# Kernel tuning notes

Hardware: AMD Instinct MI355X
Metric: run time of the kernel (lower is better)

## Reference

```python
import jax, jax.numpy as jnp
import numpy as np

BS, L = 4096, 20
NF, EF, TF = 128, 128, 128
DM = 3 * NF + EF + TF          # 640: attention model dim
DIN = DM - TF                  # 512: GRU input dim
NHEAD = 2
NNODES, NEDGES = 100000, 500000
ODE_STEPS = 8


def setup_inputs() -> dict:
    key = jax.random.key(0)
    ks = jax.random.split(key, 32)
    p = lambda i, shape, s: jax.random.normal(ks[i], shape, dtype=jnp.float32) * s
    return {
        'nids': jax.random.randint(ks[0], (BS,), 1, NNODES),
        'ts': jax.random.uniform(ks[1], (BS,), dtype=jnp.float32),
        'hist_nids': jax.random.randint(ks[2], (BS, L), 0, NNODES),
        'anonymized_ids': jax.random.randint(ks[3], (BS, L), 0, L + 1),
        'hist_eids': jax.random.randint(ks[4], (BS, L), 0, NEDGES),
        'hist_ts': jnp.sort(jax.random.uniform(ks[5], (BS, L), dtype=jnp.float32), axis=1),
        'hist_dirs': jax.random.randint(ks[6], (BS, L), 0, 2),
        'node_feat': p(7, (NNODES, NF), 0.1),
        'edge_feat': p(8, (NEDGES, EF), 0.1),
        'anony_emb': p(9, (L + 1, NF), 0.1),
        'time_w': p(10, (TF,), 1.0),
        'time_b': p(11, (TF,), 1.0),
        'in_proj_w': p(12, (3 * DM, DM), 0.02),
        'in_proj_b': jnp.zeros((3 * DM,), jnp.float32),
        'out_proj_w': p(13, (DM, DM), 0.02),
        'out_proj_b': jnp.zeros((DM,), jnp.float32),
        'outfn_w': p(14, (NF, DM), 0.02),
        'outfn_b': jnp.zeros((NF,), jnp.float32),
        'attn_wq': p(15, (NF, NF), 0.05),
        'attn_wk': p(16, (NF + EF + TF, NF), 0.05),
        'attn_wv': p(17, (NF + EF + TF, NF), 0.05),
        'merge_w': p(18, (2 * NF, NF), 0.05),
        'merge_b': jnp.zeros((NF,), jnp.float32),
        'gru_w_ih': p(19, (3 * NF, DIN), 0.05),
        'gru_w_hh': p(20, (3 * NF, NF), 0.05),
        'gru_b_ih': jnp.zeros((3 * NF,), jnp.float32),
        'gru_b_hh': jnp.zeros((3 * NF,), jnp.float32),
        'ode_w': p(21, (NF, NF), 0.05),
        'ode_b': jnp.zeros((NF,), jnp.float32),
        'tnode_w': p(22, (NF,), 1.0),
        'tnode_b': p(23, (NF,), 1.0),
    }


def reference(nids, ts, hist_nids, anonymized_ids, hist_eids, hist_ts, hist_dirs,
              node_feat, edge_feat, anony_emb, time_w, time_b,
              in_proj_w, in_proj_b, out_proj_w, out_proj_b, outfn_w, outfn_b,
              attn_wq, attn_wk, attn_wv, merge_w, merge_b,
              gru_w_ih, gru_w_hh, gru_b_ih, gru_b_hh,
              ode_w, ode_b, tnode_w, tnode_b):
    bs, hl = hist_nids.shape
    mask = (hist_nids == 0)
    mask = mask.at[:, -1].set(False)
    invalid_rows = jnp.all(mask, axis=1, keepdims=True)  # [bs,1]

    r_nids = jnp.broadcast_to(nids[:, None], (bs, hl))
    src_nids = r_nids * hist_dirs + hist_nids * (1 - hist_dirs)
    dst_nids = r_nids * (1 - hist_dirs) + hist_nids * hist_dirs

    src_vals = node_feat[src_nids]                 # [bs,L,NF] gather
    dst_vals = node_feat[dst_nids]                 # [bs,L,NF] gather
    edge_vals = edge_feat[hist_eids]               # [bs,L,EF] gather
    anony_vals = anony_emb[anonymized_ids]         # [bs,L,NF] gather
    dt = hist_ts[:, -1:] - hist_ts                 # [bs,L]
    ts_vals = jnp.cos(dt[..., None] * time_w + time_b)  # [bs,L,TF] TimeEncode

    full_vals = jnp.concatenate([src_vals, dst_vals, anony_vals, edge_vals, ts_vals], axis=2)
    last_event_feat = full_vals[:, -1, :DIN]
    full_vals = full_vals.at[:, -1, :DIN].set(0.0)

    # --- self MHA over history (nn.MultiheadAttention with key_padding_mask) ---
    qkv = full_vals @ in_proj_w.T + in_proj_b      # [bs,L,3*DM]
    q, k, v = jnp.split(qkv, 3, axis=-1)
    dh = DM // NHEAD
    rs = lambda x: x.reshape(bs, hl, NHEAD, dh)
    scores = jnp.einsum('blhd,bmhd->bhlm', rs(q), rs(k)) / np.sqrt(dh)
    scores = jnp.where(mask[:, None, None, :], -1e9, scores)
    attn = jax.nn.softmax(scores, axis=-1)
    ctx = jnp.einsum('bhlm,bmhd->blhd', attn, rs(v)).reshape(bs, hl, DM)
    mha_out = ctx @ out_proj_w.T + out_proj_b

    # --- temporal graph attention embedding (GraphAttnEmbedding stand-in) ---
    qn = mha_out[:, -1] @ outfn_w.T + outfn_b      # [bs,NF]
    nb = jnp.concatenate([node_feat[hist_nids], edge_vals, ts_vals], axis=2)  # [bs,L,NF+EF+TF]
    qh = qn @ attn_wq                              # [bs,NF]
    kh = nb @ attn_wk                              # [bs,L,NF]
    vh = nb @ attn_wv                              # [bs,L,NF]
    sc = jnp.einsum('bd,bld->bl', qh, kh) / np.sqrt(NF)
    sc = jnp.where(mask, -1e9, sc)
    a = jax.nn.softmax(sc, axis=-1)
    ctx2 = jnp.einsum('bl,bld->bd', a, vh)
    h_prev_left = jnp.tanh(jnp.concatenate([ctx2, node_feat[nids]], axis=1) @ merge_w + merge_b)

    # --- GRUCell jump update ---
    gi = last_event_feat @ gru_w_ih.T + gru_b_ih
    gh = h_prev_left @ gru_w_hh.T + gru_b_hh
    ir, iz, inn = jnp.split(gi, 3, axis=-1)
    hr, hz, hn = jnp.split(gh, 3, axis=-1)
    r = jax.nn.sigmoid(ir + hr)
    zg = jax.nn.sigmoid(iz + hz)
    n = jnp.tanh(inn + r * hn)
    h_prev_right = (1.0 - zg) * n + zg * h_prev_left

    # --- neural ODE transform (RK4 over s in [0,1]) ---
    t0 = hist_ts[:, -2:-1]                         # prev_prev_ts [bs,1]
    t1 = hist_ts[:, -1:]                           # prev_ts      [bs,1]
    ratio = t1 - t0                                # (end-start)=1.0

    def f(s, z):
        t = s * ratio + t0                         # [bs,1]
        te = jnp.cos(t * tnode_w + tnode_b)        # [bs,NF]
        return jnp.tanh((z + te) @ ode_w.T + ode_b) * ratio

    ds = 1.0 / ODE_STEPS

    def step(z, s):
        k1 = f(s, z)
        k2 = f(s + 0.5 * ds, z + 0.5 * ds * k1)
        k3 = f(s + 0.5 * ds, z + 0.5 * ds * k2)
        k4 = f(s + ds, z + ds * k3)
        return z + (ds / 6.0) * (k1 + 2 * k2 + 2 * k3 + k4), None

    h_left, _ = jax.lax.scan(step, h_prev_right, jnp.arange(ODE_STEPS, dtype=jnp.float32) * ds)

    h_left = jnp.where(invalid_rows, 0.0, h_left)
    h_right = jnp.where(invalid_rows, 0.0, h_prev_right)
    return h_left, h_right, hist_ts[:, -1]
```

## Files before the change

kernel.cpp:

```cpp
#include <hip/hip_runtime.h>
#include <math.h>

#define BSZ 4096
#define HL  20
#define NF  128
#define DM  640
#define DIN 512
#define DH  320

static __device__ __forceinline__ float sigmoidf_(float x){ return 1.f/(1.f+expf(-x)); }
static __device__ __forceinline__ unsigned short f2b_(float v){
    return (unsigned short)((__float_as_uint(v) + 0x8000u) >> 16);
}
static __device__ __forceinline__ float b2f_(unsigned short u){
    return __uint_as_float(((unsigned int)u) << 16);
}

__global__ void k_comb(const float* __restrict__ outfn_w,
                       const float* __restrict__ out_proj_w,
                       float* __restrict__ combT)
{
    int jc = blockIdx.x, jq = threadIdx.x;
    float acc = 0.f;
    for (int e = 0; e < DM; ++e)
        acc += outfn_w[jq*DM + e] * out_proj_w[e*DM + jc];
    combT[jc*NF + jq] = acc;
}

__global__ void k_zz(const float* __restrict__ in_proj_w,
                     const float* __restrict__ combT,
                     float* __restrict__ ZZ)
{
    int ef = blockIdx.x;
    int h = ef / DM, e = ef - h*DM;
    int jq = threadIdx.x;
    const float* wv = in_proj_w + (2*DM + h*DH)*DM + e;
    const float* cb = combT + (h*DH)*NF + jq;
    float acc = 0.f;
    for (int dd = 0; dd < DH; ++dd)
        acc += wv[dd*DM] * cb[dd*NF];
    ZZ[ef*NF + jq] = acc;
}

__global__ void k_qbias(const float* __restrict__ outfn_b,
                        const float* __restrict__ out_proj_b,
                        const float* __restrict__ outfn_w,
                        const float* __restrict__ in_proj_b,
                        const float* __restrict__ combT,
                        float* __restrict__ qb)
{
    int jq = threadIdx.x;
    float acc = outfn_b[jq];
    for (int e = 0; e < DM; ++e)  acc += out_proj_b[e] * outfn_w[jq*DM + e];
    for (int jc = 0; jc < DM; ++jc) acc += in_proj_b[2*DM + jc] * combT[jc*NF + jq];
    qb[jq] = acc;
}

__global__ void k_transpose(const float* __restrict__ gih,
                            const float* __restrict__ ghh,
                            float* __restrict__ giT,
                            float* __restrict__ ghT)
{
    int i = blockIdx.x*blockDim.x + threadIdx.x;
    if (i < DIN*3*NF) {
        int d = i / (3*NF), j = i - d*(3*NF);
        giT[i] = gih[j*DIN + d];
    } else {
        int i2 = i - DIN*3*NF;
        int d = i2 / (3*NF), j = i2 - d*(3*NF);
        ghT[i2] = ghh[j*NF + d];
    }
}

__global__ void k_qc(const float* __restrict__ time_b,
                     const float* __restrict__ in_proj_w,
                     const float* __restrict__ in_proj_b,
                     float* __restrict__ qcv)
{
    __shared__ float tsr[NF];
    int tid = threadIdx.x;
    tsr[tid] = cosf(time_b[tid]);
    __syncthreads();
    int j = blockIdx.x*128 + tid;
    const float* wr = in_proj_w + j*DM + DIN;
    float acc = in_proj_b[j];
    for (int d = 0; d < NF; ++d) acc += tsr[d]*wr[d];
    qcv[j] = acc;
}

__global__ void k_cc(const float* __restrict__ qcv,
                     const float* __restrict__ in_proj_b,
                     float* __restrict__ cc)
{
    int wave = threadIdx.x >> 6, lane = threadIdx.x & 63;
    float acc = 0.f;
    for (int j = lane; j < DH; j += 64)
        acc += qcv[wave*DH + j] * in_proj_b[DM + wave*DH + j];
    for (int off = 32; off > 0; off >>= 1) acc += __shfl_down(acc, off);
    if (lane == 0) cc[wave] = acc;
}

__global__ void k_u(const float* __restrict__ qcv,
                    const float* __restrict__ in_proj_w,
                    float* __restrict__ u)
{
    int d = blockIdx.x*64 + threadIdx.x;
    int h = d / DM, dd = d - h*DM;
    const float* base = in_proj_w + (DM + h*DH)*DM + dd;
    const float* q = qcv + h*DH;
    float acc = 0.f;
    for (int j = 0; j < DH; ++j) acc += q[j]*base[j*DM];
    u[d] = acc;
}

__global__ __launch_bounds__(256) void k_attn1(
    const int* __restrict__ nids, const int* __restrict__ hist_nids,
    const int* __restrict__ aidsp, const int* __restrict__ eidsp,
    const float* __restrict__ hist_ts, const int* __restrict__ dirsp,
    const float* __restrict__ node_feat, const float* __restrict__ edge_feat,
    const float* __restrict__ anony_emb,
    const float* __restrict__ time_w, const float* __restrict__ time_b,
    const float* __restrict__ u, const float* __restrict__ cc,
    float* __restrict__ wbuf, float* __restrict__ lef)
{
    int b = blockIdx.x, tid = threadIdx.x;
    int wave = tid >> 6, lane = tid & 63;
    __shared__ unsigned short zh[HL][DM];
    __shared__ float ul[2*DM];
    __shared__ float sc[2][HL];
    __shared__ float aw[2][HL];
    __shared__ int   shn[HL], sdir[HL], said[HL], seid[HL];
    __shared__ float sts[HL];

    if (tid < HL) {
        shn[tid]  = hist_nids[b*HL+tid];
        sdir[tid] = dirsp[b*HL+tid];
        said[tid] = aidsp[b*HL+tid];
        seid[tid] = eidsp[b*HL+tid];
        sts[tid]  = hist_ts[b*HL+tid];
    }
    for (int i = tid; i < 2*DM; i += 256) ul[i] = u[i];
    float twA = time_w[lane],    tbA = time_b[lane];
    float twB = time_w[64+lane], tbB = time_b[64+lane];
    __syncthreads();

    float ulr0[10], ulr1[10];
    #pragma unroll
    for (int s = 0; s < 10; ++s) {
        ulr0[s] = ul[s*64 + lane];
        ulr1[s] = ul[DM + s*64 + lane];
    }

    int rnid = nids[b];
    float tlast = sts[HL-1];

    int srcv[5], dstv[5], aidv[5], eidv[5];
    float dtv[5];
    #pragma unroll
    for (int r = 0; r < 5; ++r) {
        int l = wave + 4*r;
        int hn = shn[l], dir = sdir[l];
        srcv[r] = dir ? rnid : hn;
        dstv[r] = dir ? hn : rnid;
        aidv[r] = said[l];
        eidv[r] = eidv[r] = seid[l];
        dtv[r]  = tlast - sts[l];
    }
    float zr[5][10];
    #pragma unroll
    for (int r = 0; r < 5; ++r) {
        zr[r][0] = node_feat[srcv[r]*NF + lane];
        zr[r][1] = node_feat[srcv[r]*NF + 64 + lane];
        zr[r][2] = node_feat[dstv[r]*NF + lane];
        zr[r][3] = node_feat[dstv[r]*NF + 64 + lane];
        zr[r][4] = anony_emb[aidv[r]*NF + lane];
        zr[r][5] = anony_emb[aidv[r]*NF + 64 + lane];
        zr[r][6] = edge_feat[eidv[r]*NF + lane];
        zr[r][7] = edge_feat[eidv[r]*NF + 64 + lane];
        zr[r][8] = cosf(dtv[r]*twA + tbA);
        zr[r][9] = cosf(dtv[r]*twB + tbB);
    }
    float c0 = cc[0], c1 = cc[1];
    #pragma unroll
    for (int r = 0; r < 5; ++r) {
        int l = wave + 4*r;
        if (l == HL-1) {
            #pragma unroll
            for (int s = 0; s < 8; ++s) {
                lef[b*DIN + s*64 + lane] = zr[r][s];
                zr[r][s] = 0.f;
            }
        }
        float d0 = 0.f, d1 = 0.f;
        #pragma unroll
        for (int s = 0; s < 10; ++s) {
            float v = zr[r][s];
            d0 += ulr0[s]*v;
            d1 += ulr1[s]*v;
            zh[l][s*64 + lane] = f2b_(v);
        }
        for (int off = 32; off > 0; off >>= 1) {
            d0 += __shfl_down(d0, off);
            d1 += __shfl_down(d1, off);
        }
        if (lane == 0) {
            bool msk = (shn[l] == 0) && (l != HL-1);
            sc[0][l] = msk ? -1.0e9f : (d0 + c0)*0.05590169943749474f;
            sc[1][l] = msk ? -1.0e9f : (d1 + c1)*0.05590169943749474f;
        }
    }
    __syncthreads();
    if (tid < 2) {
        float mx = -3.0e38f;
        for (int m = 0; m < HL; ++m) mx = fmaxf(mx, sc[tid][m]);
        float sum = 0.f;
        for (int m = 0; m < HL; ++m) { float e = expf(sc[tid][m]-mx); aw[tid][m] = e; sum += e; }
        float inv = 1.f/sum;
        for (int m = 0; m < HL; ++m) aw[tid][m] *= inv;
    }
    __syncthreads();
    #pragma unroll
    for (int i = tid; i < 2*DM; i += 256) {
        int h = i / DM, d = i - h*DM;
        float acc = 0.f;
        #pragma unroll
        for (int m = 0; m < HL; ++m) acc += aw[h][m]*b2f_(zh[m][d]);
        wbuf[b*2*DM + i] = acc;
    }
}

__global__ __launch_bounds__(256) void k_gemm_qn(const float* __restrict__ A,
                                                 const float* __restrict__ BT,
                                                 const float* __restrict__ bias,
                                                 float* __restrict__ C)
{
    constexpr int K = 2*DM;
    __shared__ float As[8*K];
    int r0 = blockIdx.x*8, tid = threadIdx.x;
    for (int i = tid; i < 8*K; i += 256) As[i] = A[r0*K + i];
    __syncthreads();
    int j = tid & (NF-1), rh = tid >> 7;
    const float* bp = BT + j;
    const float* ap = As + rh*4*K;
    float acc0=0.f, acc1=0.f, acc2=0.f, acc3=0.f;
    for (int d = 0; d < K; ++d) {
        float bv = bp[d*NF];
        acc0 += ap[d]*bv;
        acc1 += ap[K + d]*bv;
        acc2 += ap[2*K + d]*bv;
        acc3 += ap[3*K + d]*bv;
    }
    float bsv = bias[j];
    int rb = r0 + rh*4;
    C[(rb+0)*NF + j] = acc0 + bsv;
    C[(rb+1)*NF + j] = acc1 + bsv;
    C[(rb+2)*NF + j] = acc2 + bsv;
    C[(rb+3)*NF + j] = acc3 + bsv;
}

__global__ __launch_bounds__(256) void k_gemm_gi(const float* __restrict__ A,
                                                 const float* __restrict__ BT,
                                                 const float* __restrict__ bias,
                                                 float* __restrict__ C)
{
    constexpr int K = DIN;
    constexpr int N = 3*NF;
    __shared__ float As[8*K];
    int r0 = blockIdx.x*8, tid = threadIdx.x;
    for (int i = tid; i < 8*K; i += 256) As[i] = A[r0*K + i];
    __syncthreads();
    int j0 = tid, j1 = tid + 256;
    bool has1 = (j1 < N);
    float a0[8] = {0,0,0,0,0,0,0,0};
    float a1[8] = {0,0,0,0,0,0,0,0};
    for (int d = 0; d < K; ++d) {
        float b0 = BT[d*N + j0];
        float b1 = 0.f;
        if (has1) b1 = BT[d*N + j1];
        #pragma unroll
        for (int r = 0; r < 8; ++r) {
            float av = As[r*K + d];
            a0[r] += av*b0;
            a1[r] += av*b1;
        }
    }
    float bs0 = bias[j0];
    for (int r = 0; r < 8; ++r) C[(r0+r)*N + j0] = a0[r] + bs0;
    if (has1) {
        float bs1 = bias[j1];
        for (int r = 0; r < 8; ++r) C[(r0+r)*N + j1] = a1[r] + bs1;
    }
}

__global__ __launch_bounds__(128) void k_attn2(
    const int* __restrict__ nids, const int* __restrict__ hist_nids,
    const int* __restrict__ eidsp, const float* __restrict__ hist_ts,
    const float* __restrict__ node_feat, const float* __restrict__ edge_feat,
    const float* __restrict__ time_w, const float* __restrict__ time_b,
    const float* __restrict__ attn_wq, const float* __restrict__ attn_wk,
    const float* __restrict__ attn_wv,
    const float* __restrict__ merge_w, const float* __restrict__ merge_b,
    const float* __restrict__ qn, const float* __restrict__ gi,
    const float* __restrict__ ghT, const float* __restrict__ gru_b_hh,
    float* __restrict__ hpr_out, float* __restrict__ out)
{
    int b = blockIdx.x, tid = threadIdx.x;
    __shared__ float qns[NF], qh[NF], p[3*NF], nbar[3*NF];
    __shared__ float scl[HL], al[HL];
    __shared__ float ctx2[NF], hpl[NF], nfn[NF];
    __shared__ int   shn[HL], seid[HL];
    __shared__ float sts[HL];

    if (tid < HL) {
        shn[tid]  = hist_nids[b*HL+tid];
        seid[tid] = eidsp[b*HL+tid];
        sts[tid]  = hist_ts[b*HL+tid];
    }
    qns[tid] = qn[b*NF + tid];
    nfn[tid] = node_feat[nids[b]*NF + tid];
    __syncthreads();

    float tlast = sts[HL-1];
    {
        float acc = 0.f;
        for (int d = 0; d < NF; ++d) acc += qns[d]*attn_wq[d*NF + tid];
        qh[tid] = acc;
    }
    __syncthreads();
    for (int dd = tid; dd < 3*NF; dd += NF) {
        const float4* row4 = (const float4*)(attn_wk + dd*NF);
        float acc = 0.f;
        #pragma unroll
        for (int q4 = 0; q4 < NF/4; ++q4) {
            float4 w4 = row4[q4];
            acc += w4.x*qh[4*q4] + w4.y*qh[4*q4+1] + w4.z*qh[4*q4+2] + w4.w*qh[4*q4+3];
        }
        p[dd] = acc;
    }
    __syncthreads();
    int wave = tid >> 6, lane = tid & 63;
    for (int l = wave; l < HL; l += 2) {
        int hn = shn[l], eid = seid[l];
        float dt = tlast - sts[l];
        float acc = 0.f;
        #pragma unroll
        for (int kk = 0; kk < 6; ++kk) {
            int d = lane + 64*kk;
            float v;
            if (d < NF)            v = node_feat[hn*NF + d];
            else if (d < 2*NF)     v = edge_feat[eid*NF + (d-NF)];
            else { int dd = d-2*NF; v = cosf(dt*time_w[dd] + time_b[dd]); }
            acc += p[d]*v;
        }
        for (int off = 32; off > 0; off >>= 1) acc += __shfl_down(acc, off);
        if (lane == 0) {
            bool msk = (hn == 0) && (l != HL-1);
            scl[l] = msk ? -1.0e9f : acc*0.08838834764831845f;
        }
    }
    __syncthreads();
    if (tid == 0) {
        float mx = -3.0e38f;
        for (int m = 0; m < HL; ++m) mx = fmaxf(mx, scl[m]);
        float sum = 0.f;
        for (int m = 0; m < HL; ++m) { float e = expf(scl[m]-mx); al[m] = e; sum += e; }
        float inv = 1.f/sum;
        for (int m = 0; m < HL; ++m) al[m] *= inv;
    }
    __syncthreads();
    {
        float twj = time_w[tid], tbj = time_b[tid];
        float an = 0.f, ae = 0.f, at = 0.f;
        #pragma unroll
        for (int l = 0; l < HL; ++l) {
            float a = al[l];
            an += a*node_feat[shn[l]*NF + tid];
            ae += a*edge_feat[seid[l]*NF + tid];
            at += a*cosf((tlast - sts[l])*twj + tbj);
        }
        nbar[tid]       = an;
        nbar[tid+NF]    = ae;
        nbar[tid+2*NF]  = at;
    }
    __syncthreads();
    {
        float acc = 0.f;
        for (int d = 0; d < 3*NF; ++d) acc += nbar[d]*attn_wv[d*NF + tid];
        ctx2[tid] = acc;
    }
    __syncthreads();
    {
        float acc = merge_b[tid];
        for (int d = 0; d < NF; ++d) acc += ctx2[d]*merge_w[d*NF + tid];
        for (int d = 0; d < NF; ++d) acc += nfn[d]*merge_w[(NF+d)*NF + tid];
        hpl[tid] = tanhf(acc);
    }
    __syncthreads();
    float ghv[3];
    #pragma unroll
    for (int s = 0; s < 3; ++s) {
        int jj = s*NF + tid;
        float acc = gru_b_hh[jj];
        for (int d = 0; d < NF; ++d) acc += hpl[d]*ghT[d*3*NF + jj];
        ghv[s] = acc;
    }
    float gi0 = gi[b*3*NF + tid];
    float gi1 = gi[b*3*NF + NF + tid];
    float gi2 = gi[b*3*NF + 2*NF + tid];
    float r_ = sigmoidf_(gi0 + ghv[0]);
    float z_ = sigmoidf_(gi1 + ghv[1]);
    float n_ = tanhf(gi2 + r_*ghv[2]);
    float hpr = (1.f - z_)*n_ + z_*hpl[tid];
    out[BSZ*NF + b*NF + tid] = hpr;
    hpr_out[b*NF + tid] = hpr;
    if (tid == 0) out[2*BSZ*NF + b] = tlast;
}

#define ZPITCH 68
#define BPITCH (2*ZPITCH)

static __device__ __forceinline__ void ode_eval_pair(
    float y0, float y1,
    const float4* __restrict__ wr,
    float ob, float rat0, float rat1,
    float* __restrict__ zrow,
    int j, int h, float* k0, float* k1)
{
    int wslot = (j >> 6)*ZPITCH + (j & 63);
    if (h == 0) zrow[wslot]          = y0;
    else        zrow[BPITCH + wslot] = y1;
    __syncthreads();
    const float4* zA = (const float4*)(zrow + h*ZPITCH);
    const float4* zB = (const float4*)(zrow + BPITCH + h*ZPITCH);
    float a0 = 0.f, b0 = 0.f, a1 = 0.f, b1 = 0.f;
    #pragma unroll
    for (int q = 0; q < 16; q += 2) {
        float4 w0 = wr[q],  w1 = wr[q+1];
        float4 xA0 = zA[q], xA1 = zA[q+1];
        float4 xB0 = zB[q], xB1 = zB[q+1];
        a0 += w0.x*xA0.x + w0.y*xA0.y + w0.z*xA0.z + w0.w*xA0.w;
        b0 += w1.x*xA1.x + w1.y*xA1.y + w1.z*xA1.z + w1.w*xA1.w;
        a1 += w0.x*xB0.x + w0.y*xB0.y + w0.z*xB0.z + w0.w*xB0.w;
        b1 += w1.x*xB1.x + w1.y*xB1.y + w1.z*xB1.z + w1.w*xB1.w;
    }
    float s0 = a0 + b0, s1 = a1 + b1;
    s0 += __shfl_xor(s0, 1);
    s1 += __shfl_xor(s1, 1);
    *k0 = tanhf(s0 + ob)*rat0;
    *k1 = tanhf(s1 + ob)*rat1;
}

__global__ __launch_bounds__(256) void k_ode(
    const float* __restrict__ hpr, const float* __restrict__ hist_ts,
    const float* __restrict__ ode_w, const float* __restrict__ ode_b,
    const float* __restrict__ tnode_w, const float* __restrict__ tnode_b,
    float* __restrict__ out)
{
    __shared__ float zb[2][2*BPITCH];
    int tid = threadIdx.x;
    int j = tid >> 1, h = tid & 1;
    int b0 = blockIdx.x*2;

    float4 wr[16];
    const float4* wp = (const float4*)(ode_w + j*NF + h*64);
    #pragma unroll
    for (int i = 0; i < 16; ++i) wr[i] = wp[i];
    float twj = tnode_w[j], tbj = tnode_b[j], obj = ode_b[j];

    float z0, z1, t00, t01, rat0, rat1;
    {
        float t1a = hist_ts[(b0+0)*HL + (HL-1)];
        float t1b = hist_ts[(b0+1)*HL + (HL-1)];
        t00 = hist_ts[(b0+0)*HL + (HL-2)];
        t01 = hist_ts[(b0+1)*HL + (HL-2)];
        rat0 = t1a - t00; rat1 = t1b - t01;
        z0 = hpr[(b0+0)*NF + j];
        z1 = hpr[(b0+1)*NF + j];
    }

    float teA0 = cosf(t00*twj + tbj);
    float teA1 = cosf(t01*twj + tbj);
    #pragma unroll 1
    for (int stp = 0; stp < 8; ++stp) {
        float s0 = stp*0.125f;
        float teB0 = cosf(((s0 + 0.0625f)*rat0 + t00)*twj + tbj);
        float teB1 = cosf(((s0 + 0.0625f)*rat1 + t01)*twj + tbj);
        float teC0 = cosf(((s0 + 0.125f)*rat0 + t00)*twj + tbj);
        float teC1 = cosf(((s0 + 0.125f)*rat1 + t01)*twj + tbj);
        float k10, k11, k20, k21, k30, k31, k40, k41;
        ode_eval_pair(z0 + teA0,               z1 + teA1,               wr, obj, rat0, rat1, zb[0], j, h, &k10, &k11);
        ode_eval_pair(z0 + 0.0625f*k10 + teB0, z1 + 0.0625f*k11 + teB1, wr, obj, rat0, rat1, zb[1], j, h, &k20, &k21);
        ode_eval_pair(z0 + 0.0625f*k20 + teB0, z1 + 0.0625f*k21 + teB1, wr, obj, rat0, rat1, zb[0], j, h, &k30, &k31);
        ode_eval_pair(z0 + 0.125f*k30 + teC0,  z1 + 0.125f*k31 + teC1,  wr, obj, rat0, rat1, zb[1], j, h, &k40, &k41);
        z0 += (0.125f/6.f)*(k10 + 2.f*k20 + 2.f*k30 + k40);
        z1 += (0.125f/6.f)*(k11 + 2.f*k21 + 2.f*k31 + k41);
        teA0 = teC0; teA1 = teC1;
    }
    if (h == 0) {
        out[(b0+0)*NF + j] = z0;
        out[(b0+1)*NF + j] = z1;
    }
}

extern "C" void kernel_launch(void* const* d_in, const int* in_sizes, int n_in,
                              void* d_out, int out_size, void* d_ws, size_t ws_size,
                              hipStream_t stream)
{
    (void)in_sizes; (void)n_in; (void)out_size; (void)ws_size;
    const int*   nids      = (const int*)d_in[0];
    const int*   hist_nids = (const int*)d_in[2];
    const int*   aids      = (const int*)d_in[3];
    const int*   eids      = (const int*)d_in[4];
    const float* hist_ts   = (const float*)d_in[5];
    const int*   dirs      = (const int*)d_in[6];
    const float* node_feat = (const float*)d_in[7];
    const float* edge_feat = (const float*)d_in[8];
    const float* anony_emb = (const float*)d_in[9];
    const float* time_w    = (const float*)d_in[10];
    const float* time_b    = (const float*)d_in[11];
    const float* in_proj_w = (const float*)d_in[12];
    const float* in_proj_b = (const float*)d_in[13];
    const float* out_proj_w= (const float*)d_in[14];
    const float* out_proj_b= (const float*)d_in[15];
    const float* outfn_w   = (const float*)d_in[16];
    const float* outfn_b   = (const float*)d_in[17];
    const float* attn_wq   = (const float*)d_in[18];
    const float* attn_wk   = (const float*)d_in[19];
    const float* attn_wv   = (const float*)d_in[20];
    const float* merge_w   = (const float*)d_in[21];
    const float* merge_b   = (const float*)d_in[22];
    const float* gru_w_ih  = (const float*)d_in[23];
    const float* gru_w_hh  = (const float*)d_in[24];
    const float* gru_b_ih  = (const float*)d_in[25];
    const float* gru_b_hh  = (const float*)d_in[26];
    const float* ode_w     = (const float*)d_in[27];
    const float* ode_b     = (const float*)d_in[28];
    const float* tnode_w   = (const float*)d_in[29];
    const float* tnode_b   = (const float*)d_in[30];
    float* out = (float*)d_out;

    float* ws    = (float*)d_ws;
    float* qc    = ws;
    float* cc    = ws + 640;
    float* u     = ws + 768;
    float* wbuf  = ws + 2048;
    float* lef   = wbuf + BSZ*2*DM;
    float* qn    = lef + BSZ*DIN;
    float* gi    = qn + BSZ*NF;
    float* combT = gi + BSZ*3*NF;
    float* ZZ    = combT + DM*NF;
    float* qb    = ZZ + 2*DM*NF;
    float* giT   = qb + NF;
    float* ghT   = giT + DIN*3*NF;
    float* hpr   = wbuf;

    k_comb<<<DM, NF, 0, stream>>>(outfn_w, out_proj_w, combT);
    k_zz<<<2*DM, NF, 0, stream>>>(in_proj_w, combT, ZZ);
    k_qbias<<<1, NF, 0, stream>>>(outfn_b, out_proj_b, outfn_w, in_proj_b, combT, qb);
    k_transpose<<<960, 256, 0, stream>>>(gru_w_ih, gru_w_hh, giT, ghT);
    k_qc<<<5, 128, 0, stream>>>(time_b, in_proj_w, in_proj_b, qc);
    k_cc<<<1, 128, 0, stream>>>(qc, in_proj_b, cc);
    k_u<<<HL, 64, 0, stream>>>(qc, in_proj_w, u);

    k_attn1<<<BSZ, 256, 0, stream>>>(nids, hist_nids, aids, eids, hist_ts, dirs,
                                     node_feat, edge_feat, anony_emb,
                                     time_w, time_b, u, cc, wbuf, lef);
    k_gemm_qn<<<BSZ/8, 256, 0, stream>>>(wbuf, ZZ, qb, qn);
    k_gemm_gi<<<BSZ/8, 256, 0, stream>>>(lef, giT, gru_b_ih, gi);
    k_attn2<<<BSZ, 128, 0, stream>>>(nids, hist_nids, eids, hist_ts,
                                     node_feat, edge_feat, time_w, time_b,
                                     attn_wq, attn_wk, attn_wv, merge_w, merge_b,
                                     qn, gi, ghT, gru_b_hh, hpr, out);
    k_ode<<<BSZ/2, 256, 0, stream>>>(hpr, hist_ts, ode_w, ode_b,
                                     tnode_w, tnode_b, out);
}
```

Measured before the change: 1.006 ms.

## Fold attention weight products and split attn2 into batched GEMM, gather, tail kernels

Precomputes Wq·Wk^T (W1) and Wv·merge_w (W2) so the per-row key projection and value/merge chain collapse into single matmuls. The old per-row attn2 kernel becomes a batched GEMM for p, a gather/softmax kernel producing attention-weighted feature sums, and a tail kernel that processes 4 rows per block so merge and GRU weights are reused across rows. The goal is to cut redundant per-row weight streaming and matvec latency. The cost is two extra small prep kernels, more launches, and intermediate buffers round-tripped through global memory.

New measurement: 952.3 us. 5.4% less time.

```diff
diff --git a/kernel.cpp b/kernel.cpp
--- a/kernel.cpp
+++ b/kernel.cpp
@@ -111,6 +111,28 @@
     float acc = 0.f;
     for (int j = 0; j < DH; ++j) acc += q[j]*base[j*DM];
     u[d] = acc;
+}
+
+__global__ void k_w1(const float* __restrict__ attn_wq,
+                     const float* __restrict__ attn_wk,
+                     float* __restrict__ W1)
+{
+    int dd = blockIdx.x, d = threadIdx.x;
+    float acc = 0.f;
+    for (int t = 0; t < NF; ++t)
+        acc += attn_wq[d*NF + t] * attn_wk[dd*NF + t];
+    W1[d*3*NF + dd] = acc;
+}
+
+__global__ void k_w2(const float* __restrict__ attn_wv,
+                     const float* __restrict__ merge_w,
+                     float* __restrict__ W2)
+{
+    int d = blockIdx.x, j = threadIdx.x;
+    float acc = 0.f;
+    for (int q = 0; q < NF; ++q)
+        acc += attn_wv[d*NF + q] * merge_w[q*NF + j];
+    W2[d*NF + j] = acc;
 }
 
 __global__ __launch_bounds__(256) void k_attn1(
@@ -292,22 +314,49 @@
     }
 }
 
-__global__ __launch_bounds__(128) void k_attn2(
-    const int* __restrict__ nids, const int* __restrict__ hist_nids,
-    const int* __restrict__ eidsp, const float* __restrict__ hist_ts,
+__global__ __launch_bounds__(256) void k_gemm_p(const float* __restrict__ A,
+                                                const float* __restrict__ BT,
+                                                float* __restrict__ C)
+{
+    constexpr int K = NF;
+    constexpr int N = 3*NF;
+    __shared__ float As[8*K];
+    int r0 = blockIdx.x*8, tid = threadIdx.x;
+    for (int i = tid; i < 8*K; i += 256) As[i] = A[r0*K + i];
+    __syncthreads();
+    int j0 = tid, j1 = tid + 256;
+    bool has1 = (j1 < N);
+    float a0[8] = {0,0,0,0,0,0,0,0};
+    float a1[8] = {0,0,0,0,0,0,0,0};
+    for (int d = 0; d < K; ++d) {
+        float b0 = BT[d*N + j0];
+        float b1 = 0.f;
+        if (has1) b1 = BT[d*N + j1];
+        #pragma unroll
+        for (int r = 0; r < 8; ++r) {
+            float av = As[r*K + d];
+            a0[r] += av*b0;
+            a1[r] += av*b1;
+        }
+    }
+    for (int r = 0; r < 8; ++r) C[(r0+r)*N + j0] = a0[r];
+    if (has1) {
+        for (int r = 0; r < 8; ++r) C[(r0+r)*N + j1] = a1[r];
+    }
+}
+
+__global__ __launch_bounds__(256) void k_attn2b(
+    const int* __restrict__ hist_nids, const int* __restrict__ eidsp,
+    const float* __restrict__ hist_ts,
     const float* __restrict__ node_feat, const float* __restrict__ edge_feat,
     const float* __restrict__ time_w, const float* __restrict__ time_b,
-    const float* __restrict__ attn_wq, const float* __restrict__ attn_wk,
-    const float* __restrict__ attn_wv,
-    const float* __restrict__ merge_w, const float* __restrict__ merge_b,
-    const float* __restrict__ qn, const float* __restrict__ gi,
-    const float* __restrict__ ghT, const float* __restrict__ gru_b_hh,
-    float* __restrict__ hpr_out, float* __restrict__ out)
+    const float* __restrict__ p_all,
+    float* __restrict__ nbar_out)
 {
     int b = blockIdx.x, tid = threadIdx.x;
-    __shared__ float qns[NF], qh[NF], p[3*NF], nbar[3*NF];
+    int wave = tid >> 6, lane = tid & 63;
+    __shared__ float p[3*NF];
     __shared__ float scl[HL], al[HL];
-    __shared__ float ctx2[NF], hpl[NF], nfn[NF];
     __shared__ int   shn[HL], seid[HL];
     __shared__ float sts[HL];
 
@@ -316,30 +365,11 @@
         seid[tid] = eidsp[b*HL+tid];
         sts[tid]  = hist_ts[b*HL+tid];
     }
-    qns[tid] = qn[b*NF + tid];
-    nfn[tid] = node_feat[nids[b]*NF + tid];
+    for (int i = tid; i < 3*NF; i += 256) p[i] = p_all[b*3*NF + i];
     __syncthreads();
 
     float tlast = sts[HL-1];
-    {
-        float acc = 0.f;
-        for (int d = 0; d < NF; ++d) acc += qns[d]*attn_wq[d*NF + tid];
-        qh[tid] = acc;
-    }
-    __syncthreads();
-    for (int dd = tid; dd < 3*NF; dd += NF) {
-        const float4* row4 = (const float4*)(attn_wk + dd*NF);
-        float acc = 0.f;
-        #pragma unroll
-        for (int q4 = 0; q4 < NF/4; ++q4) {
-            float4 w4 = row4[q4];
-            acc += w4.x*qh[4*q4] + w4.y*qh[4*q4+1] + w4.z*qh[4*q4+2] + w4.w*qh[4*q4+3];
-        }
-        p[dd] = acc;
-    }
-    __syncthreads();
-    int wave = tid >> 6, lane = tid & 63;
-    for (int l = wave; l < HL; l += 2) {
+    for (int l = wave; l < HL; l += 4) {
         int hn = shn[l], eid = seid[l];
         float dt = tlast - sts[l];
         float acc = 0.f;
@@ -368,52 +398,94 @@
         for (int m = 0; m < HL; ++m) al[m] *= inv;
     }
     __syncthreads();
-    {
-        float twj = time_w[tid], tbj = time_b[tid];
-        float an = 0.f, ae = 0.f, at = 0.f;
-        #pragma unroll
-        for (int l = 0; l < HL; ++l) {
-            float a = al[l];
-            an += a*node_feat[shn[l]*NF + tid];
-            ae += a*edge_feat[seid[l]*NF + tid];
-            at += a*cosf((tlast - sts[l])*twj + tbj);
-        }
-        nbar[tid]       = an;
-        nbar[tid+NF]    = ae;
-        nbar[tid+2*NF]  = at;
-    }
-    __syncthreads();
-    {
+    for (int i = tid; i < 3*NF; i += 256) {
         float acc = 0.f;
-        for (int d = 0; d < 3*NF; ++d) acc += nbar[d]*attn_wv[d*NF + tid];
-        ctx2[tid] = acc;
-    }
-    __syncthreads();
-    {
-        float acc = merge_b[tid];
-        for (int d = 0; d < NF; ++d) acc += ctx2[d]*merge_w[d*NF + tid];
-        for (int d = 0; d < NF; ++d) acc += nfn[d]*merge_w[(NF+d)*NF + tid];
-        hpl[tid] = tanhf(acc);
-    }
-    __syncthreads();
-    float ghv[3];
-    #pragma unroll
-    for (int s = 0; s < 3; ++s) {
-        int jj = s*NF + tid;
-        float acc = gru_b_hh[jj];
-        for (int d = 0; d < NF; ++d) acc += hpl[d]*ghT[d*3*NF + jj];
-        ghv[s] = acc;
-    }
-    float gi0 = gi[b*3*NF + tid];
-    float gi1 = gi[b*3*NF + NF + tid];
-    float gi2 = gi[b*3*NF + 2*NF + tid];
-    float r_ = sigmoidf_(gi0 + ghv[0]);
-    float z_ = sigmoidf_(gi1 + ghv[1]);
-    float n_ = tanhf(gi2 + r_*ghv[2]);
-    float hpr = (1.f - z_)*n_ + z_*hpl[tid];
-    out[BSZ*NF + b*NF + tid] = hpr;
-    hpr_out[b*NF + tid] = hpr;
-    if (tid == 0) out[2*BSZ*NF + b] = tlast;
+        if (i < NF) {
+            #pragma unroll
+            for (int l = 0; l < HL; ++l) acc += al[l]*node_feat[shn[l]*NF + i];
+        } else if (i < 2*NF) {
+            int d = i - NF;
+            #pragma unroll
+            for (int l = 0; l < HL; ++l) acc += al[l]*edge_feat[seid[l]*NF + d];
+        } else {
+            int d = i - 2*NF;
+            float twj = time_w[d], tbj = time_b[d];
+            #pragma unroll
+            for (int l = 0; l < HL; ++l) acc += al[l]*cosf((tlast - sts[l])*twj + tbj);
+        }
+        nbar_out[b*3*NF + i] = acc;
+    }
+}
+
+__global__ __launch_bounds__(256) void k_tail(
+    const int* __restrict__ nids, const float* __restrict__ hist_ts,
+    const float* __restrict__ node_feat,
+    const float* __restrict__ nbar,
+    const float* __restrict__ gi,
+    const float* __restrict__ W2,
+    const float* __restrict__ merge_w,
+    const float* __restrict__ merge_b,
+    const float* __restrict__ ghT,
+    const float* __restrict__ gru_b_hh,
+    float* __restrict__ hpr_out, float* __restrict__ out)
+{
+    constexpr int R = 4;
+    __shared__ float S[R*3*NF];
+    __shared__ float F[R*NF];
+    __shared__ float Hp[R*NF];
+    __shared__ int   nid4[R];
+    int r0 = blockIdx.x*R, tid = threadIdx.x;
+    if (tid < R) nid4[tid] = nids[r0+tid];
+    __syncthreads();
+    for (int i = tid; i < R*3*NF; i += 256) S[i] = nbar[r0*3*NF + i];
+    for (int i = tid; i < R*NF; i += 256) {
+        int r = i >> 7, d = i & 127;
+        F[i] = node_feat[nid4[r]*NF + d];
+    }
+    __syncthreads();
+    int j = tid & 127, rh = tid >> 7;
+    float acc0 = merge_b[j], acc1 = acc0;
+    const float* S0 = S + (rh*2+0)*3*NF;
+    const float* S1 = S + (rh*2+1)*3*NF;
+    for (int d = 0; d < 3*NF; ++d) {
+        float w = W2[d*NF + j];
+        acc0 += S0[d]*w;
+        acc1 += S1[d]*w;
+    }
+    const float* F0 = F + (rh*2+0)*NF;
+    const float* F1 = F + (rh*2+1)*NF;
+    for (int d = 0; d < NF; ++d) {
+        float w = merge_w[(NF+d)*NF + j];
+        acc0 += F0[d]*w;
+        acc1 += F1[d]*w;
+    }
+    Hp[(rh*2+0)*NF + j] = tanhf(acc0);
+    Hp[(rh*2+1)*NF + j] = tanhf(acc1);
+    __syncthreads();
+    #pragma unroll
+    for (int q = 0; q < 2; ++q) {
+        int r = rh*2 + q;
+        const float* hp = Hp + r*NF;
+        float g0 = gru_b_hh[j], g1 = gru_b_hh[NF+j], g2 = gru_b_hh[2*NF+j];
+        for (int d = 0; d < NF; ++d) {
+            float hv = hp[d];
+            g0 += hv*ghT[d*3*NF + j];
+            g1 += hv*ghT[d*3*NF + NF + j];
+            g2 += hv*ghT[d*3*NF + 2*NF + j];
+        }
+        int rb = r0 + r;
+        float gi0 = gi[rb*3*NF + j];
+        float gi1 = gi[rb*3*NF + NF + j];
+        float gi2 = gi[rb*3*NF + 2*NF + j];
+        float hplv = hp[j];
+        float r_ = sigmoidf_(gi0 + g0);
+        float z_ = sigmoidf_(gi1 + g1);
+        float n_ = tanhf(gi2 + r_*g2);
+        float hpr = (1.f - z_)*n_ + z_*hplv;
+        out[BSZ*NF + rb*NF + j] = hpr;
+        hpr_out[rb*NF + j] = hpr;
+    }
+    if (tid < R) out[2*BSZ*NF + r0 + tid] = hist_ts[(r0+tid)*HL + (HL-1)];
 }
 
 #define ZPITCH 68
@@ -552,7 +624,11 @@
     float* qb    = ZZ + 2*DM*NF;
     float* giT   = qb + NF;
     float* ghT   = giT + DIN*3*NF;
-    float* hpr   = wbuf;
+    float* W1    = ghT + NF*3*NF;
+    float* W2    = W1 + NF*3*NF;
+    float* p_all = lef;
+    float* nbar  = wbuf;
+    float* hpr   = wbuf + BSZ*3*NF;
 
     k_comb<<<DM, NF, 0, stream>>>(outfn_w, out_proj_w, combT);
     k_zz<<<2*DM, NF, 0, stream>>>(in_proj_w, combT, ZZ);
@@ -561,16 +637,21 @@
     k_qc<<<5, 128, 0, stream>>>(time_b, in_proj_w, in_proj_b, qc);
     k_cc<<<1, 128, 0, stream>>>(qc, in_proj_b, cc);
     k_u<<<HL, 64, 0, stream>>>(qc, in_proj_w, u);
+    k_w1<<<3*NF, NF, 0, stream>>>(attn_wq, attn_wk, W1);
+    k_w2<<<3*NF, NF, 0, stream>>>(attn_wv, merge_w, W2);
 
     k_attn1<<<BSZ, 256, 0, stream>>>(nids, hist_nids, aids, eids, hist_ts, dirs,
                                      node_feat, edge_feat, anony_emb,
                                      time_w, time_b, u, cc, wbuf, lef);
     k_gemm_qn<<<BSZ/8, 256, 0, stream>>>(wbuf, ZZ, qb, qn);
     k_gemm_gi<<<BSZ/8, 256, 0, stream>>>(lef, giT, gru_b_ih, gi);
-    k_attn2<<<BSZ, 128, 0, stream>>>(nids, hist_nids, eids, hist_ts,
-                                     node_feat, edge_feat, time_w, time_b,
-                                     attn_wq, attn_wk, attn_wv, merge_w, merge_b,
-                                     qn, gi, ghT, gru_b_hh, hpr, out);
+    k_gemm_p<<<BSZ/8, 256, 0, stream>>>(qn, W1, p_all);
+    k_attn2b<<<BSZ, 256, 0, stream>>>(hist_nids, eids, hist_ts,
+                                      node_feat, edge_feat, time_w, time_b,
+                                      p_all, nbar);
+    k_tail<<<BSZ/4, 256, 0, stream>>>(nids, hist_ts, node_feat, nbar, gi,
+                                      W2, merge_w, merge_b, ghT, gru_b_hh,
+                                      hpr, out);
     k_ode<<<BSZ/2, 256, 0, stream>>>(hpr, hist_ts, ode_w, ode_b,
                                      tnode_w, tnode_b, out);
 }
```
